# Kernel tuning notes

Hardware: AMD Instinct MI355X
Metric: run time of the kernel (lower is better)

## Reference

```python
import jax, jax.numpy as jnp
import numpy as np

B, T, HID = 2, 512, 1024
H, D, K = 16, 64, 4          # heads, head_dim, short-conv kernel
P = H * D                    # projection_dim
E, TOPK, I, IS = 8, 2, 768, 768  # experts, top_k, expert inter, shared inter
EPS = 1e-5


def setup_inputs() -> dict:
    key = jax.random.key(0)
    ks = jax.random.split(key, 24)
    def r(i, shape, s=0.02):
        return jax.random.normal(ks[i], shape, jnp.float32) * s
    return {
        "x": jax.random.normal(ks[0], (B, T, HID), jnp.float32),
        "norm1_w": jnp.ones((HID,), jnp.float32),
        "wq": r(1, (HID, P)), "wk": r(2, (HID, P)), "wv": r(3, (HID, P)),
        "cq": r(4, (P, K), 0.5), "ck": r(5, (P, K), 0.5), "cv": r(6, (P, K), 0.5),
        "fa": r(7, (HID, D)), "fb": r(8, (D, P)), "bp": r(9, (HID, H)),
        "ga": r(10, (HID, D)), "gb": r(11, (D, P)),
        "A_log": jnp.log(jax.random.uniform(ks[12], (H, 1), jnp.float32, 1.0, 16.0)),
        "dt_bias": r(13, (H, D), 0.1),
        "onorm_w": jnp.ones((D,), jnp.float32),
        "wo": r(14, (P, HID)),
        "norm2_w": jnp.ones((HID,), jnp.float32),
        "gate_w": r(15, (HID, E)), "gate_b": r(16, (E,), 0.1),
        "wg_e": r(17, (E, HID, I)), "wu_e": r(18, (E, HID, I)), "wd_e": r(19, (E, I, HID)),
        "wg_s": r(20, (HID, IS)), "wu_s": r(21, (HID, IS)), "wd_s": r(22, (IS, HID)),
    }


def _rms(x, w, eps=EPS):
    return x * jax.lax.rsqrt(jnp.mean(x * x, axis=-1, keepdims=True) + eps) * w


def _dwconv_silu(x, w):
    # causal depthwise conv, NLC layout: out[b,t,c] = sum_k w[c,k] * x[b, t-(K-1)+k, c]
    xp = jnp.pad(x, ((0, 0), (K - 1, 0), (0, 0)))
    out = sum(w[:, k] * xp[:, k:k + x.shape[1], :] for k in range(K))
    return jax.nn.silu(out)


def _delta_attn(x, wq, wk, wv, cq, ck, cv, fa, fb, bp, ga, gb, A_log, dt_bias, onorm_w, wo):
    q = _dwconv_silu(x @ wq, cq).reshape(B, T, H, D)
    k = _dwconv_silu(x @ wk, ck).reshape(B, T, H, D)
    v = _dwconv_silu(x @ wv, cv).reshape(B, T, H, D)
    # L2-style rms normalization of q/k (no weight, eps=1e-6), then asymmetric scaling
    q = q * jax.lax.rsqrt(jnp.mean(q * q, -1, keepdims=True) + 1e-6)
    k = k * jax.lax.rsqrt(jnp.mean(k * k, -1, keepdims=True) + 1e-6)
    scale = float(D) ** -0.5
    q = (scale ** 2) * q
    k = scale * k
    # fine-grained per-channel gated decay + per-head write strength
    a = ((x @ fa) @ fb).reshape(B, T, H, D)
    g = jnp.exp(-jnp.exp(A_log)[None, None] * jax.nn.softplus(a + dt_bias))  # (B,T,H,D)
    beta = jax.nn.sigmoid(x @ bp)  # (B,T,H)

    def step(S, qkvgb):
        qt, kt, vt, gt, bt = qkvgb            # (B,H,D) each, bt (B,H)
        S = S * gt[..., None]                  # decay over key dim, S: (B,H,Dk,Dv)
        pred = jnp.einsum('bhk,bhkv->bhv', kt, S)
        S = S + jnp.einsum('bhk,bhv->bhkv', kt, (vt - pred) * bt[..., None])
        o = jnp.einsum('bhk,bhkv->bhv', qt, S)
        return S, o

    xs = tuple(jnp.moveaxis(t_, 1, 0) for t_ in (q, k, v, g, beta))
    S0 = jnp.zeros((B, H, D, D), x.dtype)
    _, o = jax.lax.scan(step, S0, xs)
    o = jnp.moveaxis(o, 0, 1)                  # (B,T,H,D)
    gate = ((x @ ga) @ gb).reshape(B, T, H, D)
    o = _rms(o, onorm_w) * jax.nn.sigmoid(gate)
    return o.reshape(B, T, P) @ wo


def _moe(x, gate_w, gate_b, wg_e, wu_e, wd_e, wg_s, wu_s, wd_s):
    n = x.reshape(-1, HID)                     # (N, HID)
    scores = jax.nn.sigmoid(n @ gate_w)        # sigmoid router
    biased = scores + gate_b                   # e_score_correction bias (selection only)
    _, inds = jax.lax.top_k(biased, TOPK)      # n_group==1 -> plain top-k
    w = jnp.take_along_axis(scores, inds, -1)  # gather ORIGINAL scores
    w = w / (w.sum(-1, keepdims=True) + 1e-20) # renormalize; routed_scaling=1.0
    N = n.shape[0]
    comb = jnp.zeros((N, E), n.dtype).at[jnp.arange(N)[:, None], inds].add(w)
    hg = jnp.einsum('nd,edi->eni', n, wg_e)
    hu = jnp.einsum('nd,edi->eni', n, wu_e)
    eo = jnp.einsum('eni,eih->enh', jax.nn.silu(hg) * hu, wd_e)
    routed = jnp.einsum('ne,enh->nh', comb, eo)
    shared = (jax.nn.silu(n @ wg_s) * (n @ wu_s)) @ wd_s
    return (routed + shared).reshape(x.shape)


def _forward(x, norm1_w, wq, wk, wv, cq, ck, cv, fa, fb, bp, ga, gb, A_log, dt_bias,
             onorm_w, wo, norm2_w, gate_w, gate_b, wg_e, wu_e, wd_e, wg_s, wu_s, wd_s):
    h = x + _delta_attn(_rms(x, norm1_w), wq, wk, wv, cq, ck, cv, fa, fb, bp, ga, gb,
                        A_log, dt_bias, onorm_w, wo)
    return h + _moe(_rms(h, norm2_w), gate_w, gate_b, wg_e, wu_e, wd_e, wg_s, wu_s, wd_s)


def reference(x, norm1_w, wq, wk, wv, cq, ck, cv, fa, fb, bp, ga, gb, A_log, dt_bias,
              onorm_w, wo, norm2_w, gate_w, gate_b, wg_e, wu_e, wd_e, wg_s, wu_s, wd_s):
    return _forward(x, norm1_w, wq, wk, wv, cq, ck, cv, fa, fb, bp, ga, gb, A_log,
                    dt_bias, onorm_w, wo, norm2_w, gate_w, gate_b, wg_e, wu_e, wd_e,
                    wg_s, wu_s, wd_s)
```

## Files before the change

kernel.cpp:

```cpp
#include <hip/hip_runtime.h>
#include <hip/hip_bf16.h>
#include <math.h>

#define Bb 2
#define Tt 512
#define HIDD 1024
#define Hh 16
#define Dd 64
#define Pp 1024
#define Kc 4
#define Ee 8
#define Ii 768
#define Ntok (Bb*Tt)
#define NASSIGN (2*Ntok)
#define NTOT (NASSIGN + Ntok)
#define SCH 8
#define SNCH (Tt/SCH)
#define NQKV 3200

typedef __attribute__((ext_vector_type(8))) short bf16x8;
typedef __attribute__((ext_vector_type(4))) float floatx4;

__device__ __forceinline__ float sigmoidf_(float x){ return 1.f/(1.f+expf(-x)); }
__device__ __forceinline__ float siluf_(float x){ return x/(1.f+expf(-x)); }
__device__ __forceinline__ float bf2f(__hip_bfloat16 b){ return __bfloat162float(b); }

__device__ __forceinline__ void async16(void* lds, const void* g) {
  __builtin_amdgcn_global_load_lds(
      (const __attribute__((address_space(1))) void*)g,
      (__attribute__((address_space(3))) void*)lds, 16, 0, 0);
}

template<int CTRL>
__device__ __forceinline__ float dpp_add(float x){
  int y = __builtin_amdgcn_update_dpp(0, __float_as_int(x), CTRL, 0xF, 0xF, true);
  return x + __int_as_float(y);
}

__device__ __forceinline__ void ds_read128(floatx4& d, const float* p){
  asm volatile("ds_read_b128 %0, %1"
    : "=v"(d)
    : "v"((const __attribute__((address_space(3))) float*)p));
}
__device__ __forceinline__ void ds_read32f(float& d, const float* p){
  asm volatile("ds_read_b32 %0, %1"
    : "=v"(d)
    : "v"((const __attribute__((address_space(3))) float*)p));
}

__global__ __launch_bounds__(256)
void prep_kernel(const float* __restrict__ x, const float* __restrict__ w,
                 const float* __restrict__ bp,
                 __hip_bfloat16* __restrict__ xhi, __hip_bfloat16* __restrict__ xlo,
                 float* __restrict__ betab,
                 const float* __restrict__ wq, const float* __restrict__ wk,
                 const float* __restrict__ wv, const float* __restrict__ wo,
                 const float* __restrict__ fa, const float* __restrict__ ga,
                 __hip_bfloat16* __restrict__ qkv_hi, __hip_bfloat16* __restrict__ qkv_lo,
                 __hip_bfloat16* __restrict__ wo_hi, __hip_bfloat16* __restrict__ wo_lo,
                 const float* __restrict__ fb, const float* __restrict__ gb,
                 __hip_bfloat16* __restrict__ fbgb_dst) {
  __shared__ float red[4];
  __shared__ float redb[4][16];
  __shared__ float tile[32][33];
  int bid = blockIdx.x;
  if (bid < Ntok) {
    int row = bid;
    const float* xr = x + (size_t)row*HIDD;
    float s = 0.f;
    for (int i = threadIdx.x; i < HIDD; i += 256){ float v = xr[i]; s += v*v; }
    #pragma unroll
    for (int off=32; off; off>>=1) s += __shfl_down(s, off, 64);
    if ((threadIdx.x & 63)==0) red[threadIdx.x>>6] = s;
    __syncthreads();
    float tot = red[0]+red[1]+red[2]+red[3];
    float sc = rsqrtf(tot/(float)HIDD + 1e-5f);
    float bacc[16] = {};
    for (int i = threadIdx.x; i < HIDD; i += 256) {
      float v = xr[i]*sc*w[i];
      __hip_bfloat16 h = __float2bfloat16(v);
      xhi[(size_t)row*HIDD+i] = h;
      xlo[(size_t)row*HIDD+i] = __float2bfloat16(v - bf2f(h));
      #pragma unroll
      for (int n=0;n<16;n++) bacc[n] += v * bp[i*16+n];
    }
    #pragma unroll
    for (int n=0;n<16;n++){
      #pragma unroll
      for (int off=32; off; off>>=1) bacc[n] += __shfl_down(bacc[n], off, 64);
    }
    if ((threadIdx.x & 63)==0){
      #pragma unroll
      for (int n=0;n<16;n++) redb[threadIdx.x>>6][n] = bacc[n];
    }
    __syncthreads();
    if (threadIdx.x < 16)
      betab[(size_t)row*16 + threadIdx.x] =
        sigmoidf_(redb[0][threadIdx.x]+redb[1][threadIdx.x]+redb[2][threadIdx.x]+redb[3][threadIdx.x]);
    return;
  }
  int tx = threadIdx.x & 31, ty0 = threadIdx.x >> 5;
  if (bid < Ntok + 6144) {
    int b2 = bid - Ntok;
    int z = b2 >> 10;
    int r2 = b2 & 1023;
    int n0 = (r2 & 31)*32, k0 = (r2 >> 5)*32;
    const float* src; __hip_bfloat16* hi; __hip_bfloat16* lo; int N;
    if (z < 4) {
      src = (z==0)?wq:(z==1)?wk:(z==2)?wv:wo;
      hi = (z<3) ? qkv_hi + (size_t)z*Pp*HIDD : wo_hi;
      lo = (z<3) ? qkv_lo + (size_t)z*Pp*HIDD : wo_lo;
      N = 1024;
    } else {
      if (n0 >= 64) return;
      src = (z==4) ? fa : ga;
      hi = qkv_hi + (size_t)(3072 + (z-4)*64)*HIDD;
      lo = qkv_lo + (size_t)(3072 + (z-4)*64)*HIDD;
      N = 64;
    }
    #pragma unroll
    for (int j=0;j<4;j++){ int ty = ty0 + j*8; tile[ty][tx] = src[(size_t)(k0+ty)*N + n0+tx]; }
    __syncthreads();
    #pragma unroll
    for (int j=0;j<4;j++){
      int ty = ty0 + j*8;
      float v = tile[tx][ty];
      __hip_bfloat16 h = __float2bfloat16(v);
      hi[(size_t)(n0+ty)*HIDD + k0+tx] = h;
      lo[(size_t)(n0+ty)*HIDD + k0+tx] = __float2bfloat16(v - bf2f(h));
    }
    return;
  }
  int b3 = bid - Ntok - 6144;
  int z = b3 >> 6;
  int r3 = b3 & 63;
  int n0 = (r3 & 31)*32, k0 = (r3 >> 5)*32;
  const float* src = z ? gb : fb;
  #pragma unroll
  for (int j=0;j<4;j++){ int ty = ty0 + j*8; tile[ty][tx] = src[(size_t)(k0+ty)*Pp + n0+tx]; }
  __syncthreads();
  #pragma unroll
  for (int j=0;j<4;j++){
    int ty = ty0 + j*8;
    size_t row = (size_t)(z*1024 + n0+ty);
    fbgb_dst[row*128 + (z?64:0) + k0+tx] = __float2bfloat16(tile[tx][ty]);
    fbgb_dst[row*128 + (z?0:64) + k0+tx] = __float2bfloat16(0.f);
  }
}

__global__ __launch_bounds__(256)
void moe_prep_kernel(const float* __restrict__ h, const float* __restrict__ w2,
                     const float* __restrict__ gw,
                     __hip_bfloat16* __restrict__ hn, float* __restrict__ scores,
                     const float* __restrict__ wg_e, const float* __restrict__ wu_e,
                     const float* __restrict__ wg_s, const float* __restrict__ wu_s,
                     const float* __restrict__ wd_e, const float* __restrict__ wd_s,
                     __hip_bfloat16* __restrict__ up_dst, __hip_bfloat16* __restrict__ dn_dst) {
  __shared__ float red[4];
  __shared__ float red2[4][Ee];
  __shared__ float tile[32][33];
  int bid = blockIdx.x;
  if (bid < Ntok) {
    int row = bid;
    const float* hr = h + (size_t)row*HIDD;
    float s = 0.f;
    for (int i = threadIdx.x; i < HIDD; i += 256){ float v = hr[i]; s += v*v; }
    #pragma unroll
    for (int off=32; off; off>>=1) s += __shfl_down(s, off, 64);
    if ((threadIdx.x & 63)==0) red[threadIdx.x>>6] = s;
    __syncthreads();
    float sc = rsqrtf((red[0]+red[1]+red[2]+red[3])/(float)HIDD + 1e-5f);
    float acc[Ee] = {};
    for (int i = threadIdx.x; i < HIDD; i += 256){
      float xv = hr[i]*sc*w2[i];
      hn[(size_t)row*HIDD + i] = __float2bfloat16(xv);
      #pragma unroll
      for (int e=0;e<Ee;e++) acc[e] += xv*gw[i*Ee+e];
    }
    #pragma unroll
    for (int e=0;e<Ee;e++){
      #pragma unroll
      for (int off=32; off; off>>=1) acc[e] += __shfl_down(acc[e], off, 64);
    }
    if ((threadIdx.x & 63)==0){
      #pragma unroll
      for (int e=0;e<Ee;e++) red2[threadIdx.x>>6][e] = acc[e];
    }
    __syncthreads();
    if (threadIdx.x < Ee)
      scores[(size_t)row*Ee + threadIdx.x] =
        red2[0][threadIdx.x]+red2[1][threadIdx.x]+red2[2][threadIdx.x]+red2[3][threadIdx.x];
    return;
  }
  int b2 = bid - Ntok;
  int z = b2 >> 10;
  int r2 = b2 & 1023;
  int n0 = (r2 & 31)*32, k0 = (r2 >> 5)*32;
  int tx = threadIdx.x & 31, ty0 = threadIdx.x >> 5;
  if (z < 18) {
    if (n0 >= Ii) return;
    int e = z >> 1, phase = z & 1;
    const float* src = (e < 8) ? ((phase ? wu_e : wg_e) + (size_t)e*HIDD*Ii)
                               : (phase ? wu_s : wg_s);
    __hip_bfloat16* dst = up_dst + (size_t)e*(2*Ii*HIDD);
    #pragma unroll
    for (int j=0;j<4;j++){ int ty = ty0 + j*8; tile[ty][tx] = src[(size_t)(k0+ty)*Ii + n0+tx]; }
    __syncthreads();
    #pragma unroll
    for (int j=0;j<4;j++){
      int ty = ty0 + j*8;
      dst[(size_t)(2*(n0+ty)+phase)*HIDD + k0+tx] = __float2bfloat16(tile[tx][ty]);
    }
  } else {
    if (k0 >= Ii) return;
    int e = z - 18;
    const float* src = (e < 8) ? wd_e + (size_t)e*Ii*HIDD : wd_s;
    __hip_bfloat16* dst = dn_dst + (size_t)e*HIDD*Ii;
    #pragma unroll
    for (int j=0;j<4;j++){ int ty = ty0 + j*8; tile[ty][tx] = src[(size_t)(k0+ty)*HIDD + n0+tx]; }
    __syncthreads();
    #pragma unroll
    for (int j=0;j<4;j++){ int ty = ty0 + j*8; dst[(size_t)(n0+ty)*Ii + k0+tx] = __float2bfloat16(tile[tx][ty]); }
  }
}

__device__ __forceinline__ int lds_off(int row, int slot){
  return row*128 + (((slot ^ row)&7)<<4);
}

template<int MODE, int ACC, int BND>
__global__ __launch_bounds__(256)
void gemm_k(const __hip_bfloat16* __restrict__ A, const __hip_bfloat16* __restrict__ BT,
            void* __restrict__ C, int M, int N, int K, int lda, const float* __restrict__ resid,
            const int* __restrict__ counts, const int* __restrict__ prefix,
            const int* __restrict__ ctok, const int* __restrict__ cslot,
            const float* __restrict__ cwt) {
  constexpr int NF = BND/32;
  int Me = M;
  int moff = 0;
  if (MODE == 4 || MODE == 6) {
    int e = blockIdx.z;
    Me = counts[e]; moff = prefix[e];
    if (MODE == 4) A += (size_t)moff * lda;
    BT += (size_t)e * (size_t)N * K;
  }
  int row0 = blockIdx.y * 64;
  if (row0 >= Me) return;
  int col0 = blockIdx.x * BND;

  __shared__ __attribute__((aligned(16))) short As[64*64];
  __shared__ __attribute__((aligned(16))) short Bs[BND*64];
  __shared__ int sidx[64];
  const int lane = threadIdx.x & 63;
  const int w    = threadIdx.x >> 6;
  const int wr = w >> 1, wc = w & 1;
  const int srow = lane >> 3;
  const int sch  = (lane & 7) ^ (srow & 7);
  const int q = lane >> 4, r16 = lane & 15;

  if (MODE == 6) {
    if (threadIdx.x < 64) {
      int rr = row0 + threadIdx.x;
      sidx[threadIdx.x] = (rr < Me) ? ctok[moff + rr] : 0;
    }
    __syncthreads();
  }

  const __hip_bfloat16* Ag = A  + (size_t)row0 * lda;
  const __hip_bfloat16* Bg = BT + (size_t)col0 * K;

  floatx4 acc[2][NF] = {};

  for (int k0 = 0; k0 < K; k0 += 64) {
    #pragma unroll
    for (int ii = 0; ii < 2; ++ii) {
      const int inst = w + ii*4;
      const int r = inst*8 + srow;
      if (MODE == 6)
        async16((char*)As + inst*1024, A + (size_t)sidx[r]*lda + (size_t)(k0 + sch*8));
      else
        async16((char*)As + inst*1024, Ag + (size_t)r*lda + (size_t)(k0 + sch*8));
    }
    #pragma unroll
    for (int ii = 0; ii < BND/32; ++ii) {
      const int inst = w + ii*4;
      const int r = inst*8 + srow;
      async16((char*)Bs + inst*1024, Bg + (size_t)r*K + (size_t)(k0 + sch*8));
    }
    __syncthreads();
    #pragma unroll
    for (int kk = 0; kk < 2; ++kk) {
      int slot = kk*4 + q;
      bf16x8 a0 = *(const bf16x8*)((const char*)As + lds_off(wr*32 +      r16, slot));
      bf16x8 a1 = *(const bf16x8*)((const char*)As + lds_off(wr*32 + 16 + r16, slot));
      bf16x8 b[NF];
      #pragma unroll
      for (int ni=0; ni<NF; ++ni)
        b[ni] = *(const bf16x8*)((const char*)Bs + lds_off(wc*(BND/2) + ni*16 + r16, slot));
      #pragma unroll
      for (int ni=0; ni<NF; ++ni){
        acc[0][ni] = __builtin_amdgcn_mfma_f32_16x16x32_bf16(a0, b[ni], acc[0][ni], 0, 0, 0);
        acc[1][ni] = __builtin_amdgcn_mfma_f32_16x16x32_bf16(a1, b[ni], acc[1][ni], 0, 0, 0);
      }
    }
    __syncthreads();
  }

  #pragma unroll
  for (int mi = 0; mi < 2; ++mi) {
    #pragma unroll
    for (int r = 0; r < 4; ++r) {
      int grow = row0 + wr*32 + mi*16 + q*4 + r;
      if (grow >= Me) continue;
      #pragma unroll
      for (int ni = 0; ni < NF; ++ni) {
        int gcol = col0 + wc*(BND/2) + ni*16 + r16;
        float v = acc[mi][ni][r];
        if (MODE == 4) {
          int rc = moff + grow;
          int tok = ctok[rc], sl = cslot[rc];
          ((__hip_bfloat16*)C)[((size_t)tok*3 + sl)*N + gcol] = __float2bfloat16(cwt[rc]*v);
        } else if (MODE == 6) {
          float pv = __shfl_xor(v, 1, 64);
          if ((lane & 1) == 0) {
            float rglu = siluf_(v) * pv;
            ((__hip_bfloat16*)C)[(size_t)(moff+grow)*(N/2) + (gcol>>1)] = __float2bfloat16(rglu);
          }
        } else if (MODE == 8) {
          if (gcol < 1024) {
            int hh2 = gcol >> 6, d2 = gcol & 63;
            float t2 = v + cwt[hh2*64 + d2];
            float sp = (t2 > 20.f) ? t2 : log1pf(expf(t2));
            ((float*)C)[(size_t)grow*1024 + gcol] = expf(-expf(resid[hh2]) * sp);
          } else {
            ((float*)(size_t)ctok)[(size_t)grow*1024 + (gcol-1024)] = v;
          }
        }
      }
    }
  }
}

template<int MODE, int BND>
__global__ __launch_bounds__(256)
void gemm3_k(const __hip_bfloat16* __restrict__ Ahi, const __hip_bfloat16* __restrict__ Alo,
             const __hip_bfloat16* __restrict__ Bhi, const __hip_bfloat16* __restrict__ Blo,
             float* __restrict__ C, int M, int N, int K, const float* __restrict__ resid) {
  constexpr int NF = BND/32;
  int row0 = blockIdx.y * 64;
  int col0 = blockIdx.x * BND;

  __shared__ __attribute__((aligned(16))) short As[64*64];
  __shared__ __attribute__((aligned(16))) short Bs[2][BND*64];
  const int lane = threadIdx.x & 63;
  const int w    = threadIdx.x >> 6;
  const int wr = w >> 1, wc = w & 1;
  const int srow = lane >> 3;
  const int sch  = (lane & 7) ^ (srow & 7);
  const int q = lane >> 4, r16 = lane & 15;

  const __hip_bfloat16* Ag0 = Ahi + (size_t)row0 * K;
  const __hip_bfloat16* Ag1 = Alo + (size_t)row0 * K;
  const __hip_bfloat16* Bg0 = Bhi + (size_t)col0 * K;
  const __hip_bfloat16* Bg1 = Blo + (size_t)col0 * K;

  floatx4 acc[2][NF] = {};

  for (int k0 = 0; k0 < K; k0 += 64) {
    #pragma unroll
    for (int ii = 0; ii < 2; ++ii) {
      const int inst = w + ii*4;
      const int r = inst*8 + srow;
      async16((char*)As + inst*1024, Ag0 + (size_t)r*K + (size_t)(k0 + sch*8));
    }
    #pragma unroll
    for (int ii = 0; ii < BND/32; ++ii) {
      const int inst = w + ii*4;
      const int r = inst*8 + srow;
      async16((char*)Bs[0] + inst*1024, Bg0 + (size_t)r*K + (size_t)(k0 + sch*8));
      async16((char*)Bs[1] + inst*1024, Bg1 + (size_t)r*K + (size_t)(k0 + sch*8));
    }
    __syncthreads();
    #pragma unroll
    for (int kk = 0; kk < 2; ++kk) {
      int slot = kk*4 + q;
      bf16x8 a0 = *(const bf16x8*)((const char*)As + lds_off(wr*32 +      r16, slot));
      bf16x8 a1 = *(const bf16x8*)((const char*)As + lds_off(wr*32 + 16 + r16, slot));
      #pragma unroll
      for (int pb = 0; pb < 2; ++pb) {
        bf16x8 b[NF];
        #pragma unroll
        for (int ni=0; ni<NF; ++ni)
          b[ni] = *(const bf16x8*)((const char*)Bs[pb] + lds_off(wc*(BND/2) + ni*16 + r16, slot));
        #pragma unroll
        for (int ni=0; ni<NF; ++ni){
          acc[0][ni] = __builtin_amdgcn_mfma_f32_16x16x32_bf16(a0, b[ni], acc[0][ni], 0, 0, 0);
          acc[1][ni] = __builtin_amdgcn_mfma_f32_16x16x32_bf16(a1, b[ni], acc[1][ni], 0, 0, 0);
        }
      }
    }
    __syncthreads();
  }
  for (int k0 = 0; k0 < K; k0 += 64) {
    #pragma unroll
    for (int ii = 0; ii < 2; ++ii) {
      const int inst = w + ii*4;
      const int r = inst*8 + srow;
      async16((char*)As + inst*1024, Ag1 + (size_t)r*K + (size_t)(k0 + sch*8));
    }
    #pragma unroll
    for (int ii = 0; ii < BND/32; ++ii) {
      const int inst = w + ii*4;
      const int r = inst*8 + srow;
      async16((char*)Bs[0] + inst*1024, Bg0 + (size_t)r*K + (size_t)(k0 + sch*8));
    }
    __syncthreads();
    #pragma unroll
    for (int kk = 0; kk < 2; ++kk) {
      int slot = kk*4 + q;
      bf16x8 a0 = *(const bf16x8*)((const char*)As + lds_off(wr*32 +      r16, slot));
      bf16x8 a1 = *(const bf16x8*)((const char*)As + lds_off(wr*32 + 16 + r16, slot));
      bf16x8 b[NF];
      #pragma unroll
      for (int ni=0; ni<NF; ++ni)
        b[ni] = *(const bf16x8*)((const char*)Bs[0] + lds_off(wc*(BND/2) + ni*16 + r16, slot));
      #pragma unroll
      for (int ni=0; ni<NF; ++ni){
        acc[0][ni] = __builtin_amdgcn_mfma_f32_16x16x32_bf16(a0, b[ni], acc[0][ni], 0, 0, 0);
        acc[1][ni] = __builtin_amdgcn_mfma_f32_16x16x32_bf16(a1, b[ni], acc[1][ni], 0, 0, 0);
      }
    }
    __syncthreads();
  }

  #pragma unroll
  for (int mi = 0; mi < 2; ++mi) {
    #pragma unroll
    for (int r = 0; r < 4; ++r) {
      int grow = row0 + wr*32 + mi*16 + q*4 + r;
      #pragma unroll
      for (int ni = 0; ni < NF; ++ni) {
        int gcol = col0 + wc*(BND/2) + ni*16 + r16;
        float v = acc[mi][ni][r];
        if (MODE == 3) {
          if (gcol < 3072)
            C[(size_t)grow*3072 + gcol] = v;
          else
            ((__hip_bfloat16*)(size_t)resid)[(size_t)grow*128 + (gcol-3072)] = __float2bfloat16(v);
        } else {
          if (MODE == 2) v += resid[(size_t)grow*N + gcol];
          C[(size_t)grow*N + gcol] = v;
        }
      }
    }
  }
}

__global__ void conv_norm_kernel(const float* __restrict__ in,
                                 const float* __restrict__ cq, const float* __restrict__ ck,
                                 const float* __restrict__ cv,
                                 float* __restrict__ qc, float* __restrict__ kc,
                                 float* __restrict__ vc) {
  int tok = blockIdx.x;
  int mode = blockIdx.y;
  const float* w = (mode==0) ? cq : (mode==1) ? ck : cv;
  float* outp    = (mode==0) ? qc : (mode==1) ? kc : vc;
  int colOff = mode << 10;
  int t = threadIdx.x;
  int c0 = t*4;
  int tloc = tok & (Tt-1);

  float wv[4][4];
  #pragma unroll
  for (int i=0;i<4;i++){
    float4 w4 = ((const float4*)w)[c0+i];
    wv[i][0]=w4.x; wv[i][1]=w4.y; wv[i][2]=w4.z; wv[i][3]=w4.w;
  }
  float acc[4] = {0.f,0.f,0.f,0.f};
  #pragma unroll
  for (int j=0;j<Kc;j++){
    int tt = tloc - (Kc-1) + j;
    if (tt >= 0){
      float4 xv = *(const float4*)&in[(size_t)(tok-(Kc-1)+j)*3072 + colOff + c0];
      acc[0] += wv[0][j]*xv.x;
      acc[1] += wv[1][j]*xv.y;
      acc[2] += wv[2][j]*xv.z;
      acc[3] += wv[3][j]*xv.w;
    }
  }
  float val[4];
  #pragma unroll
  for (int i=0;i<4;i++) val[i] = siluf_(acc[i]);
  float scale = 1.f;
  if (mode < 2) {
    float ss = val[0]*val[0]+val[1]*val[1]+val[2]*val[2]+val[3]*val[3];
    ss += __shfl_xor(ss, 1, 64);
    ss += __shfl_xor(ss, 2, 64);
    ss += __shfl_xor(ss, 4, 64);
    ss += __shfl_xor(ss, 8, 64);
    scale = rsqrtf(ss/(float)Dd + 1e-6f) * ((mode==0) ? (1.f/64.f) : 0.125f);
  }
  float4 o4 = make_float4(val[0]*scale, val[1]*scale, val[2]*scale, val[3]*scale);
  *(float4*)&outp[(size_t)tok*Pp + c0] = o4;
}

#define REGLOAD(bufi, tbase, K,G,Q,VV,BT) do { \
  const int _b = (bufi); const int _t0 = (tbase); \
  _Pragma("unroll") \
  for (int _i=0;_i<SCH;_i++){ \
    ds_read128(K[_i], &sk[_b][_i][kq*4]); \
    ds_read128(G[_i], &sg[_b][_i][kq*4]); \
    ds_read128(Q[_i], &sq[_b][_i][kq*4]); \
    ds_read32f(VV[_i], &sbv[_t0+_i][vi]); \
    ds_read32f(BT[_i], &sb[_t0+_i]); \
  } \
} while(0)

#define SSTEP(K,G,Q,VV,BT,_i,_t) do { \
  floatx4 k4=K[_i], g4=G[_i], q4=Q[_i]; \
  float vvv=VV[_i], bt=BT[_i]; \
  S0*=g4.x; S1*=g4.y; S2*=g4.z; S3*=g4.w; \
  float pred = S0*k4.x + S1*k4.y + S2*k4.z + S3*k4.w; \
  pred = dpp_add<0xB1>(pred); pred = dpp_add<0x4E>(pred); \
  pred = dpp_add<0x141>(pred); pred = dpp_add<0x140>(pred); \
  float upd = (vvv - pred) * bt; \
  S0 += k4.x*upd; S1 += k4.y*upd; S2 += k4.z*upd; S3 += k4.w*upd; \
  float acc = S0*q4.x + S1*q4.y + S2*q4.z + S3*q4.w; \
  acc = dpp_add<0xB1>(acc); acc = dpp_add<0x4E>(acc); \
  acc = dpp_add<0x141>(acc); acc = dpp_add<0x140>(acc); \
  if (kq == 0) so[_t][vi] = acc; \
} while(0)

#define SITER(c, KC,GC,QC,VC,BC, KN,GN,QN,VN,BN) do { \
  if ((c)+1 < SNCH) { \
    if ((c)+2 < SNCH) asm volatile("s_waitcnt vmcnt(6)" ::: "memory"); \
    else              asm volatile("s_waitcnt vmcnt(0)" ::: "memory"); \
    REGLOAD(((c)+1)%3, ((c)+1)*SCH, KN,GN,QN,VN,BN); \
    if ((c)+3 < SNCH) stage(((c)+3)*SCH, ((c)+3)%3); \
  } \
  _Pragma("unroll") \
  for (int _s=0;_s<SCH;_s++) SSTEP(KC,GC,QC,VC,BC,_s,(c)*SCH+_s); \
  asm volatile("s_waitcnt lgkmcnt(0)" ::: "memory"); \
  __builtin_amdgcn_sched_barrier(0); \
} while(0)

__global__ __launch_bounds__(64)
void scan_kernel(const float* __restrict__ q, const float* __restrict__ k,
                 const float* __restrict__ v, const float* __restrict__ g,
                 const float* __restrict__ beta, float* __restrict__ o) {
  const int vb = blockIdx.x & 15;
  const int hh = (blockIdx.x >> 4) & 15;
  const int b  = blockIdx.x >> 8;
  const int lane = threadIdx.x;
  const int kq = lane & 15;
  const int vi = lane >> 4;
  const int v0 = vb*4;
  const int rb = b*Tt;

  __shared__ __attribute__((aligned(16))) float sq[3][SCH][64];
  __shared__ __attribute__((aligned(16))) float sk[3][SCH][64];
  __shared__ __attribute__((aligned(16))) float sg[3][SCH][64];
  __shared__ __attribute__((aligned(16))) float sbv[Tt][4];
  __shared__ float sb[Tt];
  __shared__ __attribute__((aligned(16))) float so[Tt][4];

  #pragma unroll
  for (int i=0;i<Tt/64;i++)
    sb[i*64+lane] = beta[(size_t)(rb + i*64 + lane)*Hh + hh];
  asm volatile("s_waitcnt vmcnt(0)" ::: "memory");

  #pragma unroll
  for (int i=0;i<Tt/64;i++)
    async16(&sbv[i*64][0], v + (size_t)(rb + i*64 + lane)*Pp + hh*64 + v0);

  auto stage = [&](int t0, int buf) {
    const int srow = lane >> 4, sch4 = (lane & 15)*4;
    #pragma unroll
    for (int ii=0; ii<2; ++ii) {
      size_t gbase = (size_t)(rb + t0 + ii*4 + srow)*Pp + hh*64;
      async16(&sq[buf][ii*4][0], q + gbase + sch4);
      async16(&sk[buf][ii*4][0], k + gbase + sch4);
      async16(&sg[buf][ii*4][0], g + gbase + sch4);
    }
  };

  floatx4 Ka[SCH],Ga[SCH],Qa[SCH], Kb[SCH],Gb[SCH],Qb[SCH];
  float Va[SCH],Bta[SCH], Vb2[SCH],Btb[SCH];
  float S0=0.f,S1=0.f,S2=0.f,S3=0.f;

  stage(0, 0);
  stage(SCH, 1);
  asm volatile("s_waitcnt vmcnt(6)" ::: "memory");
  REGLOAD(0, 0, Ka,Ga,Qa,Va,Bta);
  stage(2*SCH, 2);
  asm volatile("s_waitcnt lgkmcnt(0)" ::: "memory");
  __builtin_amdgcn_sched_barrier(0);

  for (int cp = 0; cp < SNCH; cp += 2) {
    SITER(cp,   Ka,Ga,Qa,Va,Bta, Kb,Gb,Qb,Vb2,Btb);
    SITER(cp+1, Kb,Gb,Qb,Vb2,Btb, Ka,Ga,Qa,Va,Bta);
  }

  #pragma unroll
  for (int i=0;i<Tt/64;i++){
    int t = i*64 + lane;
    *(float4*)&o[(size_t)(rb+t)*Pp + hh*64 + v0] = *(const float4*)&so[t][0];
  }
}

__global__ void onorm_gate_split_kernel(const float* __restrict__ o, const float* __restrict__ w,
                                        const float* __restrict__ gate,
                                        __hip_bfloat16* __restrict__ hi, __hip_bfloat16* __restrict__ lo) {
  int row = blockIdx.x*4 + (threadIdx.x>>6);
  int lane = threadIdx.x & 63;
  size_t idx = (size_t)row*Dd + lane;
  float v = o[idx];
  float s = v*v;
  #pragma unroll
  for (int off=32; off; off>>=1) s += __shfl_xor(s, off, 64);
  float r = v * rsqrtf(s/(float)Dd + 1e-5f) * w[lane] * sigmoidf_(gate[idx]);
  __hip_bfloat16 h = __float2bfloat16(r);
  hi[idx] = h;
  lo[idx] = __float2bfloat16(r - bf2f(h));
}

__global__ void router_compact_kernel(const float* __restrict__ logits, const float* __restrict__ gate_b,
                                      int* __restrict__ counts, int* __restrict__ prefix,
                                      int* __restrict__ ctok, int* __restrict__ cslot,
                                      float* __restrict__ cwt) {
  int n = threadIdx.x;
  __shared__ int scnt[Ee];
  __shared__ int spre[Ee];
  __shared__ int soff[Ee];
  if (n < Ee) { scnt[n] = 0; soff[n] = 0; }
  __syncthreads();
  float sc[Ee], bi[Ee];
  #pragma unroll
  for (int e=0;e<Ee;e++){ float s = sigmoidf_(logits[n*Ee+e]); sc[e]=s; bi[e]=s+gate_b[e]; }
  int i0=0;
  #pragma unroll
  for (int e=1;e<Ee;e++) if (bi[e] > bi[i0]) i0=e;
  int i1=-1;
  #pragma unroll
  for (int e=0;e<Ee;e++){ if (e==i0) continue; if (i1<0 || bi[e] > bi[i1]) i1=e; }
  float w0=sc[i0], w1=sc[i1];
  float inv = 1.f/(w0+w1+1e-20f);
  w0*=inv; w1*=inv;
  atomicAdd(&scnt[i0],1);
  atomicAdd(&scnt[i1],1);
  __syncthreads();
  if (n == 0){ int s=0; for (int e=0;e<Ee;e++){ spre[e]=s; s+=scnt[e]; } }
  __syncthreads();
  int p0 = spre[i0] + atomicAdd(&soff[i0],1);
  ctok[p0]=n; cslot[p0]=0; cwt[p0]=w0;
  int p1 = spre[i1] + atomicAdd(&soff[i1],1);
  ctok[p1]=n; cslot[p1]=1; cwt[p1]=w1;
  ctok[NASSIGN+n]=n; cslot[NASSIGN+n]=2; cwt[NASSIGN+n]=1.f;
  if (n < Ee){ counts[n]=scnt[n]; prefix[n]=spre[n]; }
  if (n == 0){ counts[Ee]=Ntok; prefix[Ee]=NASSIGN; }
}

__global__ void final_kernel(const float* __restrict__ h, const __hip_bfloat16* __restrict__ routed,
                             float* __restrict__ out) {
  int idx = blockIdx.x*256 + threadIdx.x;
  if (idx >= Ntok*HIDD) return;
  int n = idx >> 10, c = idx & 1023;
  const __hip_bfloat16* rp = routed + (size_t)n*3*HIDD + c;
  out[idx] = h[idx] + bf2f(rp[0]) + bf2f(rp[HIDD]) + bf2f(rp[2*HIDD]);
}

extern "C" void kernel_launch(void* const* d_in, const int* in_sizes, int n_in,
                              void* d_out, int out_size, void* d_ws, size_t ws_size,
                              hipStream_t stream) {
  (void)in_sizes; (void)n_in; (void)out_size; (void)ws_size;
  const float* x        = (const float*)d_in[0];
  const float* norm1_w  = (const float*)d_in[1];
  const float* wq       = (const float*)d_in[2];
  const float* wk       = (const float*)d_in[3];
  const float* wv       = (const float*)d_in[4];
  const float* cq       = (const float*)d_in[5];
  const float* ck       = (const float*)d_in[6];
  const float* cv       = (const float*)d_in[7];
  const float* fa       = (const float*)d_in[8];
  const float* fb       = (const float*)d_in[9];
  const float* bp       = (const float*)d_in[10];
  const float* ga       = (const float*)d_in[11];
  const float* gb       = (const float*)d_in[12];
  const float* A_log    = (const float*)d_in[13];
  const float* dt_bias  = (const float*)d_in[14];
  const float* onorm_w  = (const float*)d_in[15];
  const float* wo       = (const float*)d_in[16];
  const float* norm2_w  = (const float*)d_in[17];
  const float* gate_w   = (const float*)d_in[18];
  const float* gate_b   = (const float*)d_in[19];
  const float* wg_e     = (const float*)d_in[20];
  const float* wu_e     = (const float*)d_in[21];
  const float* wd_e     = (const float*)d_in[22];
  const float* wg_s     = (const float*)d_in[23];
  const float* wu_s     = (const float*)d_in[24];
  const float* wd_s     = (const float*)d_in[25];
  float* out = (float*)d_out;

  char* base = (char*)d_ws;
  size_t off = 0;
  auto alloc = [&](size_t bytes)->char* {
    off = (off + 255) & ~(size_t)255;
    char* p = base + off; off += bytes; return p;
  };
  float* hbuf = (float*)alloc((size_t)Ntok*HIDD*4);
  size_t uStart = (off + 255) & ~(size_t)255;

  off = uStart;
  __hip_bfloat16* xn      = (__hip_bfloat16*)alloc((size_t)Ntok*HIDD*2);
  __hip_bfloat16* xn_lo   = (__hip_bfloat16*)alloc((size_t)Ntok*HIDD*2);
  __hip_bfloat16* wqkv_t  = (__hip_bfloat16*)alloc((size_t)NQKV*HIDD*2);
  __hip_bfloat16* wqkv_lo = (__hip_bfloat16*)alloc((size_t)NQKV*HIDD*2);
  float*          qkvlin  = (float*)alloc((size_t)Ntok*3*Pp*4);
  float*          qc      = (float*)alloc((size_t)Ntok*Pp*4);
  float*          kc      = (float*)alloc((size_t)Ntok*Pp*4);
  float*          vc      = (float*)alloc((size_t)Ntok*Pp*4);
  float*          gbuf    = (float*)alloc((size_t)Ntok*Pp*4);
  float*          gatebuf = (float*)alloc((size_t)Ntok*Pp*4);
  float*          obuf    = (float*)alloc((size_t)Ntok*Pp*4);
  __hip_bfloat16* atmp12  = (__hip_bfloat16*)alloc((size_t)Ntok*2*Dd*2);
  float*          betab   = (float*)alloc((size_t)Ntok*Hh*4);
  __hip_bfloat16* obuf_hi = (__hip_bfloat16*)alloc((size_t)Ntok*Pp*2);
  __hip_bfloat16* obuf_lo = (__hip_bfloat16*)alloc((size_t)Ntok*Pp*2);
  __hip_bfloat16* wo_t    = (__hip_bfloat16*)alloc((size_t)HIDD*Pp*2);
  __hip_bfloat16* wo_lo   = (__hip_bfloat16*)alloc((size_t)HIDD*Pp*2);
  __hip_bfloat16* fbgb_t  = (__hip_bfloat16*)alloc((size_t)2048*128*2);

  off = uStart;
  __hip_bfloat16* hn      = (__hip_bfloat16*)alloc((size_t)Ntok*HIDD*2);
  float*          scores  = (float*)alloc((size_t)Ntok*Ee*4);
  int*            counts  = (int*)alloc(64);
  int*            prefix  = (int*)alloc(64);
  int*            ctok    = (int*)alloc((size_t)(NTOT+64)*4);
  int*            cslot   = (int*)alloc((size_t)(NTOT+64)*4);
  float*          cwt     = (float*)alloc((size_t)(NTOT+64)*4);
  __hip_bfloat16* egu_t   = (__hip_bfloat16*)alloc((size_t)9*2*Ii*HIDD*2);
  __hip_bfloat16* act     = (__hip_bfloat16*)alloc((size_t)NTOT*Ii*2);
  __hip_bfloat16* routed  = (__hip_bfloat16*)alloc((size_t)Ntok*3*HIDD*2);
  __hip_bfloat16* ed_t    = (__hip_bfloat16*)alloc((size_t)9*HIDD*Ii*2);

  dim3 blk(256);

  prep_kernel<<<Ntok + 6144 + 128, blk, 0, stream>>>(x, norm1_w, bp, xn, xn_lo, betab,
                                                     wq, wk, wv, wo, fa, ga,
                                                     wqkv_t, wqkv_lo, wo_t, wo_lo,
                                                     fb, gb, fbgb_t);
  gemm3_k<3,128><<<dim3(25,16,1), blk, 0, stream>>>(xn, xn_lo, wqkv_t, wqkv_lo, qkvlin,
                                                    Ntok, NQKV, HIDD, (const float*)atmp12);
  conv_norm_kernel<<<dim3(Ntok,3,1), blk, 0, stream>>>(qkvlin, cq, ck, cv, qc, kc, vc);
  gemm_k<8,0,128><<<dim3(16,16,1), blk, 0, stream>>>(atmp12, fbgb_t, gbuf, Ntok, 2048, 128, 2*Dd,
                                                     A_log, nullptr, nullptr,
                                                     (const int*)gatebuf, nullptr, dt_bias);
  scan_kernel<<<Bb*Hh*16, dim3(64), 0, stream>>>(qc, kc, vc, gbuf, betab, obuf);
  onorm_gate_split_kernel<<<(Ntok*Hh)/4, blk, 0, stream>>>(obuf, onorm_w, gatebuf, obuf_hi, obuf_lo);
  gemm3_k<2,64><<<dim3(16,16,1), blk, 0, stream>>>(obuf_hi, obuf_lo, wo_t, wo_lo, hbuf,
                                                   Ntok, HIDD, Pp, x);

  moe_prep_kernel<<<Ntok + 27*1024, blk, 0, stream>>>(hbuf, norm2_w, gate_w, hn, scores,
                                                      wg_e, wu_e, wg_s, wu_s, wd_e, wd_s,
                                                      egu_t, ed_t);
  router_compact_kernel<<<1, dim3(1024), 0, stream>>>(scores, gate_b, counts, prefix,
                                                      ctok, cslot, cwt);
  gemm_k<6,0,128><<<dim3(12,16,9), blk, 0, stream>>>(hn, egu_t, act, Ntok, 2*Ii, HIDD, HIDD,
                                                     nullptr, counts, prefix, ctok, nullptr, nullptr);
  gemm_k<4,0,128><<<dim3(8,16,9), blk, 0, stream>>>(act, ed_t, routed, Ntok, HIDD, Ii, Ii,
                                                    nullptr, counts, prefix, ctok, cslot, cwt);

  final_kernel<<<(Ntok*HIDD+255)/256, blk, 0, stream>>>(hbuf, routed, out);
}
```

Baseline: 291.7 us.

## Fuse down-proj weight transpose into Wo GEMM launch to fill idle CUs

Replaces the gemm3_k Wo projection with a dedicated wo_down_kernel. Its first 16x16 blocks compute the split-precision (hi/lo) Wo GEMM plus residual, and the remaining blocks transpose and convert the expert down-projection weights to bf16. This moves that work out of moe_prep_kernel so the weight conversion runs alongside the small 256-block GEMM instead of lengthening the later MoE prep launch. The custom GEMM uses 64x64 tiles with a single LDS buffer and two sequential K passes, which may be slower than the previous templated kernel.

```diff
diff --git a/kernel.cpp b/kernel.cpp
--- a/kernel.cpp
+++ b/kernel.cpp
@@ -154,8 +154,7 @@
                      __hip_bfloat16* __restrict__ hn, float* __restrict__ scores,
                      const float* __restrict__ wg_e, const float* __restrict__ wu_e,
                      const float* __restrict__ wg_s, const float* __restrict__ wu_s,
-                     const float* __restrict__ wd_e, const float* __restrict__ wd_s,
-                     __hip_bfloat16* __restrict__ up_dst, __hip_bfloat16* __restrict__ dn_dst) {
+                     __hip_bfloat16* __restrict__ up_dst) {
   __shared__ float red[4];
   __shared__ float red2[4][Ee];
   __shared__ float tile[32][33];
@@ -197,30 +196,18 @@
   int r2 = b2 & 1023;
   int n0 = (r2 & 31)*32, k0 = (r2 >> 5)*32;
   int tx = threadIdx.x & 31, ty0 = threadIdx.x >> 5;
-  if (z < 18) {
-    if (n0 >= Ii) return;
-    int e = z >> 1, phase = z & 1;
-    const float* src = (e < 8) ? ((phase ? wu_e : wg_e) + (size_t)e*HIDD*Ii)
-                               : (phase ? wu_s : wg_s);
-    __hip_bfloat16* dst = up_dst + (size_t)e*(2*Ii*HIDD);
-    #pragma unroll
-    for (int j=0;j<4;j++){ int ty = ty0 + j*8; tile[ty][tx] = src[(size_t)(k0+ty)*Ii + n0+tx]; }
-    __syncthreads();
-    #pragma unroll
-    for (int j=0;j<4;j++){
-      int ty = ty0 + j*8;
-      dst[(size_t)(2*(n0+ty)+phase)*HIDD + k0+tx] = __float2bfloat16(tile[tx][ty]);
-    }
-  } else {
-    if (k0 >= Ii) return;
-    int e = z - 18;
-    const float* src = (e < 8) ? wd_e + (size_t)e*Ii*HIDD : wd_s;
-    __hip_bfloat16* dst = dn_dst + (size_t)e*HIDD*Ii;
-    #pragma unroll
-    for (int j=0;j<4;j++){ int ty = ty0 + j*8; tile[ty][tx] = src[(size_t)(k0+ty)*HIDD + n0+tx]; }
-    __syncthreads();
-    #pragma unroll
-    for (int j=0;j<4;j++){ int ty = ty0 + j*8; dst[(size_t)(n0+ty)*Ii + k0+tx] = __float2bfloat16(tile[tx][ty]); }
+  if (n0 >= Ii) return;
+  int e = z >> 1, phase = z & 1;
+  const float* src = (e < 8) ? ((phase ? wu_e : wg_e) + (size_t)e*HIDD*Ii)
+                             : (phase ? wu_s : wg_s);
+  __hip_bfloat16* dst = up_dst + (size_t)e*(2*Ii*HIDD);
+  #pragma unroll
+  for (int j=0;j<4;j++){ int ty = ty0 + j*8; tile[ty][tx] = src[(size_t)(k0+ty)*Ii + n0+tx]; }
+  __syncthreads();
+  #pragma unroll
+  for (int j=0;j<4;j++){
+    int ty = ty0 + j*8;
+    dst[(size_t)(2*(n0+ty)+phase)*HIDD + k0+tx] = __float2bfloat16(tile[tx][ty]);
   }
 }
 
@@ -451,6 +438,114 @@
           if (MODE == 2) v += resid[(size_t)grow*N + gcol];
           C[(size_t)grow*N + gcol] = v;
         }
+      }
+    }
+  }
+}
+
+__global__ __launch_bounds__(256)
+void wo_down_kernel(const __hip_bfloat16* __restrict__ Ahi, const __hip_bfloat16* __restrict__ Alo,
+                    const __hip_bfloat16* __restrict__ Bhi, const __hip_bfloat16* __restrict__ Blo,
+                    float* __restrict__ C, const float* __restrict__ resid,
+                    const float* __restrict__ wd_e, const float* __restrict__ wd_s,
+                    __hip_bfloat16* __restrict__ dn_dst) {
+  __shared__ __attribute__((aligned(16))) char smem[24576];
+  if (blockIdx.x >= 16) {
+    float (*tile)[33] = (float(*)[33])smem;
+    int flat = (blockIdx.x - 16)*16 + blockIdx.y;
+    int e = flat / 768, rem = flat - e*768;
+    int n0 = (rem & 31)*32, k0 = (rem >> 5)*32;
+    int tx = threadIdx.x & 31, ty0 = threadIdx.x >> 5;
+    const float* src = (e < 8) ? wd_e + (size_t)e*Ii*HIDD : wd_s;
+    __hip_bfloat16* dst = dn_dst + (size_t)e*HIDD*Ii;
+    #pragma unroll
+    for (int j=0;j<4;j++){ int ty = ty0 + j*8; tile[ty][tx] = src[(size_t)(k0+ty)*HIDD + n0+tx]; }
+    __syncthreads();
+    #pragma unroll
+    for (int j=0;j<4;j++){ int ty = ty0 + j*8; dst[(size_t)(n0+ty)*Ii + k0+tx] = __float2bfloat16(tile[tx][ty]); }
+    return;
+  }
+  char* As  = smem;
+  char* Bs0 = smem + 8192;
+  char* Bs1 = smem + 16384;
+  const int lane = threadIdx.x & 63;
+  const int w    = threadIdx.x >> 6;
+  const int wr = w >> 1, wc = w & 1;
+  const int srow = lane >> 3;
+  const int sch  = (lane & 7) ^ (srow & 7);
+  const int q = lane >> 4, r16 = lane & 15;
+  int row0 = blockIdx.y * 64;
+  int col0 = blockIdx.x * 64;
+  const int K = Pp, N = HIDD;
+
+  const __hip_bfloat16* Ag0 = Ahi + (size_t)row0 * K;
+  const __hip_bfloat16* Ag1 = Alo + (size_t)row0 * K;
+  const __hip_bfloat16* Bg0 = Bhi + (size_t)col0 * K;
+  const __hip_bfloat16* Bg1 = Blo + (size_t)col0 * K;
+
+  floatx4 acc[2][2] = {};
+
+  for (int k0 = 0; k0 < K; k0 += 64) {
+    #pragma unroll
+    for (int ii = 0; ii < 2; ++ii) {
+      const int inst = w + ii*4;
+      const int r = inst*8 + srow;
+      async16(As + inst*1024, Ag0 + (size_t)r*K + (size_t)(k0 + sch*8));
+      async16(Bs0 + inst*1024, Bg0 + (size_t)r*K + (size_t)(k0 + sch*8));
+      async16(Bs1 + inst*1024, Bg1 + (size_t)r*K + (size_t)(k0 + sch*8));
+    }
+    __syncthreads();
+    #pragma unroll
+    for (int kk = 0; kk < 2; ++kk) {
+      int slot = kk*4 + q;
+      bf16x8 a0 = *(const bf16x8*)(As + lds_off(wr*32 +      r16, slot));
+      bf16x8 a1 = *(const bf16x8*)(As + lds_off(wr*32 + 16 + r16, slot));
+      #pragma unroll
+      for (int pb = 0; pb < 2; ++pb) {
+        const char* Bp = pb ? Bs1 : Bs0;
+        bf16x8 b0 = *(const bf16x8*)(Bp + lds_off(wc*32 +      r16, slot));
+        bf16x8 b1 = *(const bf16x8*)(Bp + lds_off(wc*32 + 16 + r16, slot));
+        acc[0][0] = __builtin_amdgcn_mfma_f32_16x16x32_bf16(a0, b0, acc[0][0], 0, 0, 0);
+        acc[0][1] = __builtin_amdgcn_mfma_f32_16x16x32_bf16(a0, b1, acc[0][1], 0, 0, 0);
+        acc[1][0] = __builtin_amdgcn_mfma_f32_16x16x32_bf16(a1, b0, acc[1][0], 0, 0, 0);
+        acc[1][1] = __builtin_amdgcn_mfma_f32_16x16x32_bf16(a1, b1, acc[1][1], 0, 0, 0);
+      }
+    }
+    __syncthreads();
+  }
+  for (int k0 = 0; k0 < K; k0 += 64) {
+    #pragma unroll
+    for (int ii = 0; ii < 2; ++ii) {
+      const int inst = w + ii*4;
+      const int r = inst*8 + srow;
+      async16(As + inst*1024, Ag1 + (size_t)r*K + (size_t)(k0 + sch*8));
+      async16(Bs0 + inst*1024, Bg0 + (size_t)r*K + (size_t)(k0 + sch*8));
+    }
+    __syncthreads();
+    #pragma unroll
+    for (int kk = 0; kk < 2; ++kk) {
+      int slot = kk*4 + q;
+      bf16x8 a0 = *(const bf16x8*)(As + lds_off(wr*32 +      r16, slot));
+      bf16x8 a1 = *(const bf16x8*)(As + lds_off(wr*32 + 16 + r16, slot));
+      bf16x8 b0 = *(const bf16x8*)(Bs0 + lds_off(wc*32 +      r16, slot));
+      bf16x8 b1 = *(const bf16x8*)(Bs0 + lds_off(wc*32 + 16 + r16, slot));
+      acc[0][0] = __builtin_amdgcn_mfma_f32_16x16x32_bf16(a0, b0, acc[0][0], 0, 0, 0);
+      acc[0][1] = __builtin_amdgcn_mfma_f32_16x16x32_bf16(a0, b1, acc[0][1], 0, 0, 0);
+      acc[1][0] = __builtin_amdgcn_mfma_f32_16x16x32_bf16(a1, b0, acc[1][0], 0, 0, 0);
+      acc[1][1] = __builtin_amdgcn_mfma_f32_16x16x32_bf16(a1, b1, acc[1][1], 0, 0, 0);
+    }
+    __syncthreads();
+  }
+
+  #pragma unroll
+  for (int mi = 0; mi < 2; ++mi) {
+    #pragma unroll
+    for (int r = 0; r < 4; ++r) {
+      int grow = row0 + wr*32 + mi*16 + q*4 + r;
+      #pragma unroll
+      for (int ni = 0; ni < 2; ++ni) {
+        int gcol = col0 + wc*32 + ni*16 + r16;
+        C[(size_t)grow*N + gcol] = acc[mi][ni][r] + resid[(size_t)grow*N + gcol];
       }
     }
   }
@@ -738,10 +833,10 @@
   int*            ctok    = (int*)alloc((size_t)(NTOT+64)*4);
   int*            cslot   = (int*)alloc((size_t)(NTOT+64)*4);
   float*          cwt     = (float*)alloc((size_t)(NTOT+64)*4);
+  __hip_bfloat16* ed_t    = (__hip_bfloat16*)alloc((size_t)9*HIDD*Ii*2);
   __hip_bfloat16* egu_t   = (__hip_bfloat16*)alloc((size_t)9*2*Ii*HIDD*2);
   __hip_bfloat16* act     = (__hip_bfloat16*)alloc((size_t)NTOT*Ii*2);
   __hip_bfloat16* routed  = (__hip_bfloat16*)alloc((size_t)Ntok*3*HIDD*2);
-  __hip_bfloat16* ed_t    = (__hip_bfloat16*)alloc((size_t)9*HIDD*Ii*2);
 
   dim3 blk(256);
 
@@ -756,19 +851,19 @@
                                                      A_log, nullptr, nullptr,
                                                      (const int*)gatebuf, nullptr, dt_bias);
   scan_kernel<<<Bb*Hh*16, dim3(64), 0, stream>>>(qc, kc, vc, gbuf, betab, obuf);
-  onorm_gate_split_kernel<<<(Ntok*Hh)/4, blk, 0, stream>>>(obuf, onorm_w, gatebuf, obuf_hi, obuf_lo);
-  gemm3_k<2,64><<<dim3(16,16,1), blk, 0, stream>>>(obuf_hi, obuf_lo, wo_t, wo_lo, hbuf,
-                                                   Ntok, HIDD, Pp, x);
-
-  moe_prep_kernel<<<Ntok + 27*1024, blk, 0, stream>>>(hbuf, norm2_w, gate_w, hn, scores,
-                                                      wg_e, wu_e, wg_s, wu_s, wd_e, wd_s,
-                                                      egu_t, ed_t);
+  onorm_gate_split_kernel<<<(Ntok*Hh)/4, blk, 0, stream>>>(obuf, onorm_w, gatebuf,
+                                                           obuf_hi, obuf_lo);
+  wo_down_kernel<<<dim3(16+432,16,1), blk, 0, stream>>>(obuf_hi, obuf_lo, wo_t, wo_lo,
+                                                        hbuf, x, wd_e, wd_s, ed_t);
+
+  moe_prep_kernel<<<Ntok + 18*1024, blk, 0, stream>>>(hbuf, norm2_w, gate_w, hn, scores,
+                                                      wg_e, wu_e, wg_s, wu_s, egu_t);
   router_compact_kernel<<<1, dim3(1024), 0, stream>>>(scores, gate_b, counts, prefix,
                                                       ctok, cslot, cwt);
   gemm_k<6,0,128><<<dim3(12,16,9), blk, 0, stream>>>(hn, egu_t, act, Ntok, 2*Ii, HIDD, HIDD,
-                                                     nullptr, counts, prefix, ctok, nullptr, nullptr);
+                                                     nullptr, counts, prefix, ctok,
+                                                     nullptr, nullptr);
   gemm_k<4,0,128><<<dim3(8,16,9), blk, 0, stream>>>(act, ed_t, routed, Ntok, HIDD, Ii, Ii,
                                                     nullptr, counts, prefix, ctok, cslot, cwt);
-
   final_kernel<<<(Ntok*HIDD+255)/256, blk, 0, stream>>>(hbuf, routed, out);
 }
```

Result: no change. 294.6 us (+1.0%).
